# Optimization experiments

Hardware: AMD Instinct MI355X
Metric: run time of the kernel (lower is better)

The kernel has to match this reference:

```python
import jax, jax.numpy as jnp
import numpy as np

N = 100000   # nodes
E = 1600000  # edges (before self loops)
G = 256      # graphs in batch
F = 128      # feature_size
H = 128      # hidden_channels
L = 3        # num_layers - 1 GAT layers
NC1 = 10     # task1 classes
GF = 8       # graph_feature_size
EPS = 1e-5


def _bn_pack(key, C):
    kg, kb, km, kv = jax.random.split(key, 4)
    gamma = jax.random.uniform(kg, (C,), minval=0.5, maxval=1.5)
    beta = jax.random.normal(kb, (C,)) * 0.1
    mean = jax.random.normal(km, (C,)) * 0.1
    var = jax.random.uniform(kv, (C,), minval=0.5, maxval=1.5)
    return jnp.stack([gamma, beta, mean, var]).astype(jnp.float32)  # [4, C]


def setup_inputs() -> dict:
    key = jax.random.key(0)
    ks = jax.random.split(key, 24)
    x = jax.random.normal(ks[0], (N, F), dtype=jnp.float32)
    edge_index = jax.random.randint(ks[1], (2, E), 0, N)
    batch_ids = jnp.sort(jax.random.randint(ks[2], (N,), 0, G))
    graph_features = jax.random.normal(ks[3], (G, GF), dtype=jnp.float32)
    s = 0.05
    gat_W = jax.random.normal(ks[4], (L, F, H), dtype=jnp.float32) * s
    gat_att_src = jax.random.normal(ks[5], (L, H), dtype=jnp.float32) * s
    gat_att_dst = jax.random.normal(ks[6], (L, H), dtype=jnp.float32) * s
    gat_bias = jax.random.normal(ks[7], (L, H), dtype=jnp.float32) * 0.01
    bn_emb = _bn_pack(ks[8], H)
    bn_t1 = _bn_pack(ks[9], NC1)
    bn_comb = _bn_pack(ks[10], H + 5)
    fc1_w = jax.random.normal(ks[11], (H + 1, NC1), dtype=jnp.float32) * s
    fc1_b = jax.random.normal(ks[12], (NC1,), dtype=jnp.float32) * s
    fc2_w = jax.random.normal(ks[13], (H + 3, 2), dtype=jnp.float32) * s
    fc2_b = jax.random.normal(ks[14], (2,), dtype=jnp.float32) * s
    fc3a_w = jax.random.normal(ks[15], (H + 5, 4), dtype=jnp.float32) * s
    fc3a_b = jax.random.normal(ks[16], (4,), dtype=jnp.float32) * s
    fc3b_w = jax.random.normal(ks[17], (H + 5, 5), dtype=jnp.float32) * s
    fc3b_b = jax.random.normal(ks[18], (5,), dtype=jnp.float32) * s
    return dict(x=x, edge_index=edge_index, batch_ids=batch_ids,
                graph_features=graph_features, task=0,
                gat_W=gat_W, gat_att_src=gat_att_src, gat_att_dst=gat_att_dst,
                gat_bias=gat_bias, bn_emb=bn_emb, bn_t1=bn_t1, bn_comb=bn_comb,
                fc1_w=fc1_w, fc1_b=fc1_b, fc2_w=fc2_w, fc2_b=fc2_b,
                fc3a_w=fc3a_w, fc3a_b=fc3a_b, fc3b_w=fc3b_w, fc3b_b=fc3b_b)


def _bn_eval(x, pack):
    gamma, beta, mean, var = pack
    return (x - mean) * gamma * jax.lax.rsqrt(var + EPS) + beta


def _gat_layer(x, W, a_src, a_dst, b, src, dst):
    h = x @ W                              # [N, H]
    e_src = (h @ a_src)[src]               # [Etot]
    e_dst = (h @ a_dst)[dst]
    e = jax.nn.leaky_relu(e_src + e_dst, negative_slope=0.2)
    emax = jax.ops.segment_max(e, dst, num_segments=N)
    ee = jnp.exp(e - emax[dst])
    denom = jax.ops.segment_sum(ee, dst, num_segments=N)
    alpha = ee / denom[dst]                # edge softmax per destination node
    out = jax.ops.segment_sum(h[src] * alpha[:, None], dst, num_segments=N)
    return out + b


def _forward(x, edge_index, batch_ids, graph_features,
             gat_W, gat_att_src, gat_att_dst, gat_bias,
             bn_emb, bn_t1, bn_comb,
             fc1_w, fc1_b, fc2_w, fc2_b, fc3a_w, fc3a_b, fc3b_w, fc3b_b):
    loops = jnp.arange(N)
    src = jnp.concatenate([edge_index[0], loops])  # PyG GATConv adds self-loops
    dst = jnp.concatenate([edge_index[1], loops])
    for i in range(L):
        x = jax.nn.relu(_gat_layer(x, gat_W[i], gat_att_src[i], gat_att_dst[i],
                                   gat_bias[i], src, dst))
    # global mean pool over graphs
    sums = jax.ops.segment_sum(x, batch_ids, num_segments=G)
    cnt = jax.ops.segment_sum(jnp.ones((N,), x.dtype), batch_ids, num_segments=G)
    x = sums / jnp.maximum(cnt, 1.0)[:, None]
    x = _bn_eval(x, bn_emb)
    lev_lsb = graph_features[:, -1:]
    nx_feats = graph_features[:, -3:]
    out1 = jnp.concatenate([x, lev_lsb], axis=1) @ fc1_w + fc1_b
    out1 = _bn_eval(jax.nn.relu(out1), bn_t1)
    out2 = jax.nn.relu(jnp.concatenate([x, nx_feats], axis=1) @ fc2_w + fc2_b)
    pred2 = jnp.argmax(out2, axis=1)
    wf1 = graph_features[:, 2:3]
    wf2 = graph_features[:, 1:2]
    x3 = _bn_eval(jnp.concatenate([x, wf1, wf2, nx_feats], axis=1), bn_comb)
    b1 = x3 @ fc3a_w + fc3a_b              # [G, 4]
    b2 = x3 @ fc3b_w + fc3b_b              # [G, 5]
    m0 = (pred2 == 0)[:, None].astype(x.dtype)
    m1 = (pred2 == 1)[:, None].astype(x.dtype)
    out3 = jnp.concatenate([b1 * m0, b2 * m1], axis=1)  # [G, 9]
    return out1, out2, out3


def reference(x, edge_index, batch_ids, graph_features, task,
              gat_W, gat_att_src, gat_att_dst, gat_bias,
              bn_emb, bn_t1, bn_comb,
              fc1_w, fc1_b, fc2_w, fc2_b, fc3a_w, fc3a_b, fc3b_w, fc3b_b):
    return _forward(x, edge_index, batch_ids, graph_features,
                    gat_W, gat_att_src, gat_att_dst, gat_bias,
                    bn_emb, bn_t1, bn_comb,
                    fc1_w, fc1_b, fc2_w, fc2_b, fc3a_w, fc3a_b, fc3b_w, fc3b_b)
```

## Files before the change

### kernel.cpp

```cpp
#include <hip/hip_runtime.h>
#include <math.h>

#define Nn 100000
#define Ee 1600000
#define Mm (Ee + Nn)
#define Gg 256
#define EPSf 1e-5f
#define NB 391
#define EPB 4096
#define NEB 391

typedef _Float16 f16x8 __attribute__((ext_vector_type(8)));
typedef _Float16 half4_t __attribute__((ext_vector_type(4)));
typedef float f32x4 __attribute__((ext_vector_type(4)));


__global__ void k_zero(int* __restrict__ a, int n) {
  int i = blockIdx.x * 256 + threadIdx.x;
  if (i < n) a[i] = 0;
}

__global__ __launch_bounds__(256) void k_bcount(const int* __restrict__ dst,
                                                int* __restrict__ bcnt, int e) {
  __shared__ int lcnt[NB];
  int t = threadIdx.x;
  for (int i = t; i < NB; i += 256) lcnt[i] = 0;
  __syncthreads();
  int base = blockIdx.x * EPB;
  #pragma unroll
  for (int i = 0; i < 16; ++i) {
    int idx = base + i * 256 + t;
    if (idx < e) atomicAdd(&lcnt[dst[idx] >> 8], 1);
  }
  __syncthreads();
  for (int i = t; i < NB; i += 256)
    if (lcnt[i]) atomicAdd(&bcnt[i], lcnt[i]);
}

__global__ __launch_bounds__(512) void k_bscan(const int* __restrict__ bcnt,
                                               int* __restrict__ pairBase,
                                               int* __restrict__ tailA,
                                               int* __restrict__ bbase,
                                               int* __restrict__ rp) {
  __shared__ int s1[512], s2[512];
  int t = threadIdx.x;
  int c = (t < NB) ? bcnt[t] : 0;
  int nib = (t < NB) ? min(Nn - (t << 8), 256) : 0;
  s1[t] = c; s2[t] = c + nib;
  __syncthreads();
  for (int o = 1; o < 512; o <<= 1) {
    int u1 = (t >= o) ? s1[t - o] : 0;
    int u2 = (t >= o) ? s2[t - o] : 0;
    __syncthreads();
    s1[t] += u1; s2[t] += u2;
    __syncthreads();
  }
  if (t < NB) {
    pairBase[t] = s1[t] - c;
    tailA[t]    = s1[t] - c;
    bbase[t]    = s2[t] - (c + nib);
  }
  if (t == 0) rp[Nn] = Mm;
}

__global__ __launch_bounds__(256) void k_bin(const int* __restrict__ src,
                                             const int* __restrict__ dst,
                                             int* __restrict__ tailA,
                                             int2* __restrict__ pairs, int e) {
  __shared__ int lcnt[NB];
  __shared__ int lbase[NB];
  int t = threadIdx.x;
  for (int i = t; i < NB; i += 256) lcnt[i] = 0;
  __syncthreads();
  int base = blockIdx.x * EPB;
  int d[16], s[16], br[16];
  #pragma unroll
  for (int i = 0; i < 16; ++i) {
    int idx = base + i * 256 + t;
    if (idx < e) {
      d[i] = dst[idx]; s[i] = src[idx];
      br[i] = atomicAdd(&lcnt[d[i] >> 8], 1);
    } else br[i] = -1;
  }
  __syncthreads();
  for (int i = t; i < NB; i += 256)
    if (lcnt[i] > 0) lbase[i] = atomicAdd(&tailA[i], lcnt[i]);
  __syncthreads();
  #pragma unroll
  for (int i = 0; i < 16; ++i) {
    if (br[i] >= 0) {
      int b = d[i] >> 8;
      pairs[lbase[b] + br[i]] = make_int2(d[i], s[i]);
    }
  }
}

__global__ __launch_bounds__(256) void k_place(const int2* __restrict__ pairs,
                                               const int* __restrict__ pairBase,
                                               const int* __restrict__ bcnt,
                                               const int* __restrict__ bbase,
                                               int* __restrict__ rp,
                                               int* __restrict__ csr) {
  __shared__ int cnt[256];
  __shared__ int ofs[256];
  int b = blockIdx.x, t = threadIdx.x;
  int v0 = b << 8;
  int nib = min(Nn - v0, 256);
  int pb = pairBase[b], pc = bcnt[b];
  int cb = bbase[b];
  cnt[t] = (t < nib) ? 1 : 0;
  __syncthreads();
  for (int j = t; j < pc; j += 256) {
    int2 p = pairs[pb + j];
    atomicAdd(&cnt[p.x - v0], 1);
  }
  __syncthreads();
  int c = cnt[t];
  ofs[t] = c;
  __syncthreads();
  for (int o = 1; o < 256; o <<= 1) {
    int u = (t >= o) ? ofs[t - o] : 0;
    __syncthreads(); ofs[t] += u; __syncthreads();
  }
  int excl = ofs[t] - c;
  if (t < nib) rp[v0 + t] = cb + excl;
  cnt[t] = excl;
  __syncthreads();
  if (t < nib) {
    int pos = atomicAdd(&cnt[t], 1);
    csr[cb + pos] = v0 + t;
  }
  __syncthreads();
  for (int j = t; j < pc; j += 256) {
    int2 p = pairs[pb + j];
    int pos = atomicAdd(&cnt[p.x - v0], 1);
    csr[cb + pos] = p.y;
  }
}


__global__ void k_x2h(const float* __restrict__ X, half4_t* __restrict__ X16, int ntot4) {
  int i = blockIdx.x * 256 + threadIdx.x;
  if (i < ntot4) {
    float4 v = reinterpret_cast<const float4*>(X)[i];
    half4_t h = { (_Float16)v.x, (_Float16)v.y, (_Float16)v.z, (_Float16)v.w };
    X16[i] = h;
  }
}

__global__ void k_prepW(const float* __restrict__ W, _Float16* __restrict__ Wt) {
  int l = blockIdx.x;
  const float* w = W + (size_t)l * 16384;
  _Float16* wt = Wt + (size_t)l * 16384;
  for (int i = threadIdx.x; i < 16384; i += 256) {
    int k = i >> 7, c = i & 127;
    wt[c * 128 + k] = (_Float16)w[i];
  }
}


__global__ __launch_bounds__(256) void k_gemm(const _Float16* __restrict__ X16,
                                              const _Float16* __restrict__ Wt,
                                              const float* __restrict__ asrc,
                                              const float* __restrict__ adst,
                                              _Float16* __restrict__ H,
                                              float* __restrict__ es,
                                              float* __restrict__ ed, int n) {
  int wid = threadIdx.x >> 6;
  int lane = threadIdx.x & 63;
  int r0 = blockIdx.x * 128 + wid * 32;
  if (r0 >= n) return;
  int lo16 = lane & 15, q = lane >> 4;

  f32x4 acc0[8] = {};
  f32x4 acc1[8] = {};
  const _Float16* xb0 = X16 + (size_t)(r0 + lo16) * 128 + q * 8;
  const _Float16* xb1 = xb0 + 16 * 128;
  const _Float16* wb  = Wt + (size_t)lo16 * 128 + q * 8;

  #pragma unroll
  for (int kk = 0; kk < 4; ++kk) {
    f16x8 b0 = *reinterpret_cast<const f16x8*>(xb0 + kk * 32);
    f16x8 b1 = *reinterpret_cast<const f16x8*>(xb1 + kk * 32);
    #pragma unroll
    for (int c = 0; c < 8; ++c) {
      f16x8 a = *reinterpret_cast<const f16x8*>(wb + (size_t)c * 2048 + kk * 32);
      acc0[c] = __builtin_amdgcn_mfma_f32_16x16x32_f16(a, b0, acc0[c], 0, 0, 0);
      acc1[c] = __builtin_amdgcn_mfma_f32_16x16x32_f16(a, b1, acc1[c], 0, 0, 0);
    }
  }

  float es0 = 0.f, es1 = 0.f, ed0 = 0.f, ed1 = 0.f;
  #pragma unroll
  for (int c = 0; c < 8; ++c) {
    float4 as = reinterpret_cast<const float4*>(asrc)[c * 4 + q];
    float4 ad = reinterpret_cast<const float4*>(adst)[c * 4 + q];
    es0 += acc0[c][0] * as.x + acc0[c][1] * as.y + acc0[c][2] * as.z + acc0[c][3] * as.w;
    ed0 += acc0[c][0] * ad.x + acc0[c][1] * ad.y + acc0[c][2] * ad.z + acc0[c][3] * ad.w;
    es1 += acc1[c][0] * as.x + acc1[c][1] * as.y + acc1[c][2] * as.z + acc1[c][3] * as.w;
    ed1 += acc1[c][0] * ad.x + acc1[c][1] * ad.y + acc1[c][2] * ad.z + acc1[c][3] * ad.w;
  }
  es0 += __shfl_xor(es0, 16); es0 += __shfl_xor(es0, 32);
  ed0 += __shfl_xor(ed0, 16); ed0 += __shfl_xor(ed0, 32);
  es1 += __shfl_xor(es1, 16); es1 += __shfl_xor(es1, 32);
  ed1 += __shfl_xor(ed1, 16); ed1 += __shfl_xor(ed1, 32);

  half4_t* H4 = reinterpret_cast<half4_t*>(H);
  int row0 = r0 + lo16;
  #pragma unroll
  for (int c = 0; c < 8; ++c) {
    half4_t h0 = { (_Float16)acc0[c][0], (_Float16)acc0[c][1],
                   (_Float16)acc0[c][2], (_Float16)acc0[c][3] };
    half4_t h1 = { (_Float16)acc1[c][0], (_Float16)acc1[c][1],
                   (_Float16)acc1[c][2], (_Float16)acc1[c][3] };
    H4[(size_t)row0 * 32 + c * 4 + q]        = h0;
    H4[(size_t)(row0 + 16) * 32 + c * 4 + q] = h1;
  }
  if (lane < 16) {
    es[r0 + lane] = es0;       ed[r0 + lane] = ed0;
    es[r0 + 16 + lane] = es1;  ed[r0 + 16 + lane] = ed1;
  }
}


__global__ __launch_bounds__(256) void k_agg(const _Float16* __restrict__ H,
                                             const int* __restrict__ rp,
                                             const int* __restrict__ csr,
                                             const float* __restrict__ es,
                                             const float* __restrict__ ed,
                                             const float* __restrict__ bias,
                                             _Float16* __restrict__ Xo, int n) {
  int v = blockIdx.x * 4 + (threadIdx.x >> 6);
  if (v >= n) return;
  int lane = threadIdx.x & 63;
  int g = lane >> 4;
  int s = lane & 15;
  int r0 = rp[v], r1 = rp[v + 1];
  int deg = r1 - r0;
  float edv = ed[v];
  const f16x8* H8 = reinterpret_cast<const f16x8*>(H);
  float acc[8] = {};
  float inv;

  if (deg <= 64) {
    int u = 0;
    float e = -3.0e38f;
    if (lane < deg) {
      u = csr[r0 + lane];
      e = es[u] + edv;
      e = e > 0.f ? e : 0.2f * e;
    }
    float m = e;
    #pragma unroll
    for (int o = 32; o; o >>= 1) m = fmaxf(m, __shfl_xor(m, o));
    float pw = (lane < deg) ? __expf(e - m) : 0.f;
    float den = pw;
    #pragma unroll
    for (int o = 32; o; o >>= 1) den += __shfl_xor(den, o);
    inv = 1.f / den;
    for (int i = 0; i < deg; i += 4) {
      int idx = i + g;
      if (idx < deg) {
        int uu = __shfl(u, idx);
        float ww = __shfl(pw, idx);
        f16x8 hv = H8[(size_t)uu * 16 + s];
        #pragma unroll
        for (int k2 = 0; k2 < 8; ++k2) acc[k2] += ww * (float)hv[k2];
      }
    }
  } else {
    float m = -3.0e38f;
    for (int j = r0 + lane; j < r1; j += 64) {
      float e = es[csr[j]] + edv;
      e = e > 0.f ? e : 0.2f * e;
      m = fmaxf(m, e);
    }
    #pragma unroll
    for (int o = 32; o; o >>= 1) m = fmaxf(m, __shfl_xor(m, o));
    float den = 0.f;
    for (int j = r0 + lane; j < r1; j += 64) {
      float e = es[csr[j]] + edv;
      e = e > 0.f ? e : 0.2f * e;
      den += __expf(e - m);
    }
    #pragma unroll
    for (int o = 32; o; o >>= 1) den += __shfl_xor(den, o);
    inv = 1.f / den;
    for (int j = r0; j < r1; j += 4) {
      int idx = j + g;
      if (idx < r1) {
        int uu = csr[idx];
        float e = es[uu] + edv;
        e = e > 0.f ? e : 0.2f * e;
        float ww = __expf(e - m);
        f16x8 hv = H8[(size_t)uu * 16 + s];
        #pragma unroll
        for (int k2 = 0; k2 < 8; ++k2) acc[k2] += ww * (float)hv[k2];
      }
    }
  }
  #pragma unroll
  for (int k2 = 0; k2 < 8; ++k2) {
    acc[k2] += __shfl_xor(acc[k2], 16);
    acc[k2] += __shfl_xor(acc[k2], 32);
  }
  if (lane < 16) {
    float4 b0 = reinterpret_cast<const float4*>(bias)[s * 2];
    float4 b1 = reinterpret_cast<const float4*>(bias)[s * 2 + 1];
    f16x8 o;
    o[0] = (_Float16)fmaxf(acc[0] * inv + b0.x, 0.f);
    o[1] = (_Float16)fmaxf(acc[1] * inv + b0.y, 0.f);
    o[2] = (_Float16)fmaxf(acc[2] * inv + b0.z, 0.f);
    o[3] = (_Float16)fmaxf(acc[3] * inv + b0.w, 0.f);
    o[4] = (_Float16)fmaxf(acc[4] * inv + b1.x, 0.f);
    o[5] = (_Float16)fmaxf(acc[5] * inv + b1.y, 0.f);
    o[6] = (_Float16)fmaxf(acc[6] * inv + b1.z, 0.f);
    o[7] = (_Float16)fmaxf(acc[7] * inv + b1.w, 0.f);
    reinterpret_cast<f16x8*>(Xo)[(size_t)v * 16 + s] = o;
  }
}


__global__ __launch_bounds__(512) void k_pool(const _Float16* __restrict__ X16,
                                              const int* __restrict__ batch,
                                              const float* __restrict__ bn,
                                              float* __restrict__ xg, int n) {
  __shared__ float4 part[16][32];
  int g = blockIdx.x;
  int s = threadIdx.x & 31;
  int way = threadIdx.x >> 5;
  int lo = 0, hi = n;
  while (lo < hi) { int mid = (lo + hi) >> 1; if (batch[mid] < g) lo = mid + 1; else hi = mid; }
  int s0 = lo;
  lo = s0; hi = n;
  while (lo < hi) { int mid = (lo + hi) >> 1; if (batch[mid] < g + 1) lo = mid + 1; else hi = mid; }
  int e0 = lo;
  const half4_t* X4 = reinterpret_cast<const half4_t*>(X16);
  float4 acc = make_float4(0.f, 0.f, 0.f, 0.f);
  for (int i = s0 + way; i < e0; i += 16) {
    half4_t h = X4[(size_t)i * 32 + s];
    acc.x += (float)h[0]; acc.y += (float)h[1];
    acc.z += (float)h[2]; acc.w += (float)h[3];
  }
  part[way][s] = acc;
  __syncthreads();
  if (way == 0) {
    float4 t = part[0][s];
    #pragma unroll
    for (int w = 1; w < 16; ++w) {
      float4 u = part[w][s];
      t.x += u.x; t.y += u.y; t.z += u.z; t.w += u.w;
    }
    float invc = (e0 > s0) ? 1.f / (float)(e0 - s0) : 0.f;
    int c0 = s * 4;
    #pragma unroll
    for (int k = 0; k < 4; ++k) {
      float mean = ((const float*)&t)[k] * invc;
      int c = c0 + k;
      float gm = bn[c], bt = bn[128 + c], mu = bn[256 + c], vr = bn[384 + c];
      xg[g * 128 + c] = (mean - mu) * gm * rsqrtf(vr + EPSf) + bt;
    }
  }
}


__global__ void k_heads(const float* __restrict__ xg, const float* __restrict__ gf,
                        const float* __restrict__ bn_t1, const float* __restrict__ bn_comb,
                        const float* __restrict__ fc1w, const float* __restrict__ fc1b,
                        const float* __restrict__ fc2w, const float* __restrict__ fc2b,
                        const float* __restrict__ fc3aw, const float* __restrict__ fc3ab,
                        const float* __restrict__ fc3bw, const float* __restrict__ fc3bb,
                        float* __restrict__ out) {
  int g = blockIdx.x;
  int lane = threadIdx.x;
  __shared__ float xs[128];
  __shared__ float x3[133];
  __shared__ float o2[2];
  xs[lane] = xg[g * 128 + lane];
  xs[lane + 64] = xg[g * 128 + 64 + lane];
  __syncthreads();
  const float* gfg = &gf[g * 8];
  float lev = gfg[7];
  float nx0 = gfg[5], nx1 = gfg[6], nx2 = gfg[7];
  float wf1 = gfg[2], wf2 = gfg[1];
  if (lane < 10) {
    float o = fc1b[lane];
    for (int k = 0; k < 128; ++k) o += xs[k] * fc1w[k * 10 + lane];
    o += lev * fc1w[128 * 10 + lane];
    o = fmaxf(o, 0.f);
    float gm = bn_t1[lane], bt = bn_t1[10 + lane], mu = bn_t1[20 + lane], vr = bn_t1[30 + lane];
    out[g * 10 + lane] = (o - mu) * gm * rsqrtf(vr + EPSf) + bt;
  }
  if (lane >= 10 && lane < 12) {
    int j = lane - 10;
    float o = fc2b[j];
    for (int k = 0; k < 128; ++k) o += xs[k] * fc2w[k * 2 + j];
    o += nx0 * fc2w[128 * 2 + j] + nx1 * fc2w[129 * 2 + j] + nx2 * fc2w[130 * 2 + j];
    o = fmaxf(o, 0.f);
    o2[j] = o;
    out[2560 + g * 2 + j] = o;
  }
  for (int k = lane; k < 133; k += 64) {
    float vsrc = (k < 128) ? xs[k]
               : (k == 128) ? wf1
               : (k == 129) ? wf2
               : (k == 130) ? nx0
               : (k == 131) ? nx1 : nx2;
    float gm = bn_comb[k], bt = bn_comb[133 + k], mu = bn_comb[266 + k], vr = bn_comb[399 + k];
    x3[k] = (vsrc - mu) * gm * rsqrtf(vr + EPSf) + bt;
  }
  __syncthreads();
  bool pred1 = o2[1] > o2[0];
  if (lane < 4) {
    float o = fc3ab[lane];
    for (int k = 0; k < 133; ++k) o += x3[k] * fc3aw[k * 4 + lane];
    out[3072 + g * 9 + lane] = pred1 ? 0.f : o;
  }
  if (lane >= 4 && lane < 9) {
    int j = lane - 4;
    float o = fc3bb[j];
    for (int k = 0; k < 133; ++k) o += x3[k] * fc3bw[k * 5 + j];
    out[3072 + g * 9 + 4 + j] = pred1 ? o : 0.f;
  }
}


extern "C" void kernel_launch(void* const* d_in, const int* in_sizes, int n_in,
                              void* d_out, int out_size, void* d_ws, size_t ws_size,
                              hipStream_t stream) {
  const float* x      = (const float*)d_in[0];
  const int*   ei     = (const int*)d_in[1];
  const int*   batch  = (const int*)d_in[2];
  const float* gf     = (const float*)d_in[3];
  const float* gatW   = (const float*)d_in[5];
  const float* asrc   = (const float*)d_in[6];
  const float* adst   = (const float*)d_in[7];
  const float* gbias  = (const float*)d_in[8];
  const float* bn_emb = (const float*)d_in[9];
  const float* bn_t1  = (const float*)d_in[10];
  const float* bn_cb  = (const float*)d_in[11];
  const float* fc1w = (const float*)d_in[12]; const float* fc1b = (const float*)d_in[13];
  const float* fc2w = (const float*)d_in[14]; const float* fc2b = (const float*)d_in[15];
  const float* fc3aw = (const float*)d_in[16]; const float* fc3ab = (const float*)d_in[17];
  const float* fc3bw = (const float*)d_in[18]; const float* fc3bb = (const float*)d_in[19];
  float* out = (float*)d_out;

  char* p = (char*)d_ws;
  auto alloc = [&](size_t bytes) -> void* {
    void* r = (void*)p;
    p += (bytes + 255) & ~(size_t)255;
    return r;
  };
  _Float16* x16a = (_Float16*)alloc((size_t)Nn * 128 * 2);
  _Float16* x16b = (_Float16*)alloc((size_t)Nn * 128 * 2);
  _Float16* hbuf = (_Float16*)alloc((size_t)Nn * 128 * 2);
  _Float16* wt   = (_Float16*)alloc((size_t)3 * 16384 * 2);
  int2*  pairs = (int2*)alloc((size_t)Ee * 8);
  int*   csr  = (int*)alloc((size_t)Mm * 4);
  int*   rp   = (int*)alloc((size_t)(Nn + 1) * 4);
  int*   bcnt = (int*)alloc((size_t)NB * 4);
  int*   pairBase = (int*)alloc((size_t)NB * 4);
  int*   tailA    = (int*)alloc((size_t)NB * 4);
  int*   bbase    = (int*)alloc((size_t)NB * 4);
  float* es   = (float*)alloc((size_t)Nn * 4);
  float* ed   = (float*)alloc((size_t)Nn * 4);
  float* xg   = (float*)alloc((size_t)Gg * 128 * 4);
  if ((size_t)(p - (char*)d_ws) > ws_size) return;

  const int* srcp = ei;
  const int* dstp = ei + Ee;

  k_x2h<<<(Nn * 32 + 255) / 256, 256, 0, stream>>>(x, (half4_t*)x16a, Nn * 32);
  k_prepW<<<3, 256, 0, stream>>>(gatW, wt);

  k_zero<<<(NB + 255) / 256, 256, 0, stream>>>(bcnt, NB);
  k_bcount<<<NEB, 256, 0, stream>>>(dstp, bcnt, Ee);
  k_bscan<<<1, 512, 0, stream>>>(bcnt, pairBase, tailA, bbase, rp);
  k_bin<<<NEB, 256, 0, stream>>>(srcp, dstp, tailA, pairs, Ee);
  k_place<<<NB, 256, 0, stream>>>(pairs, pairBase, bcnt, bbase, rp, csr);

  _Float16* xin = x16a;
  _Float16* xout = x16b;
  int ngrid = (Nn + 127) / 128;
  for (int l = 0; l < 3; ++l) {
    k_gemm<<<ngrid, 256, 0, stream>>>(xin, wt + (size_t)l * 16384,
                                      asrc + l * 128, adst + l * 128,
                                      hbuf, es, ed, Nn);
    k_agg<<<(Nn + 3) / 4, 256, 0, stream>>>(hbuf, rp, csr, es, ed,
                                            gbias + l * 128, xout, Nn);
    _Float16* t = xin; xin = xout; xout = t;
  }

  k_pool<<<Gg, 512, 0, stream>>>(xin, batch, bn_emb, xg, Nn);

  k_heads<<<Gg, 64, 0, stream>>>(xg, gf, bn_t1, bn_cb,
                                 fc1w, fc1b, fc2w, fc2b, fc3aw, fc3ab, fc3bw, fc3bb, out);
}
```

Baseline: 554.4 us.

## Fuse fp32-to-fp16 conversion into first GEMM, pack edge pairs, merge pool and heads

The first GAT GEMM now reads fp32 inputs directly and converts them in registers, which removes the separate x-to-half kernel and its round trip through memory. Edge binning packs source and local destination into one 32-bit int, halving the pairs buffer traffic, and uses twice as many blocks with half the edges each. The bcount zeroing is folded into the weight-prep kernel, and pooling and heads are merged into one kernel. The aggregation loop precomputes row offsets and unrolls by two. The packing assumes src < 2^23, and the first GEMM now loads twice as many bytes per element.

```diff
diff --git a/kernel.cpp b/kernel.cpp
--- a/kernel.cpp
+++ b/kernel.cpp
@@ -7,18 +7,29 @@
 #define Gg 256
 #define EPSf 1e-5f
 #define NB 391
-#define EPB 4096
-#define NEB 391
+#define EPB 2048
+#define NEB 782
 
 typedef _Float16 f16x8 __attribute__((ext_vector_type(8)));
 typedef _Float16 half4_t __attribute__((ext_vector_type(4)));
 typedef float f32x4 __attribute__((ext_vector_type(4)));
 
 
-__global__ void k_zero(int* __restrict__ a, int n) {
-  int i = blockIdx.x * 256 + threadIdx.x;
-  if (i < n) a[i] = 0;
-}
+__global__ void k_prepW(const float* __restrict__ W, _Float16* __restrict__ Wt,
+                        int* __restrict__ bcnt) {
+  int l = blockIdx.x;
+  if (l < 3) {
+    const float* w = W + (size_t)l * 16384;
+    _Float16* wt = Wt + (size_t)l * 16384;
+    for (int i = threadIdx.x; i < 16384; i += 256) {
+      int k = i >> 7, c = i & 127;
+      wt[c * 128 + k] = (_Float16)w[i];
+    }
+  } else {
+    for (int i = threadIdx.x; i < NB; i += 256) bcnt[i] = 0;
+  }
+}
+
 
 __global__ __launch_bounds__(256) void k_bcount(const int* __restrict__ dst,
                                                 int* __restrict__ bcnt, int e) {
@@ -28,7 +39,7 @@
   __syncthreads();
   int base = blockIdx.x * EPB;
   #pragma unroll
-  for (int i = 0; i < 16; ++i) {
+  for (int i = 0; i < EPB / 256; ++i) {
     int idx = base + i * 256 + t;
     if (idx < e) atomicAdd(&lcnt[dst[idx] >> 8], 1);
   }
@@ -66,20 +77,22 @@
 __global__ __launch_bounds__(256) void k_bin(const int* __restrict__ src,
                                              const int* __restrict__ dst,
                                              int* __restrict__ tailA,
-                                             int2* __restrict__ pairs, int e) {
+                                             int* __restrict__ pairs, int e) {
   __shared__ int lcnt[NB];
   __shared__ int lbase[NB];
   int t = threadIdx.x;
   for (int i = t; i < NB; i += 256) lcnt[i] = 0;
   __syncthreads();
   int base = blockIdx.x * EPB;
-  int d[16], s[16], br[16];
-  #pragma unroll
-  for (int i = 0; i < 16; ++i) {
+  int pk[EPB / 256], br[EPB / 256], bk[EPB / 256];
+  #pragma unroll
+  for (int i = 0; i < EPB / 256; ++i) {
     int idx = base + i * 256 + t;
     if (idx < e) {
-      d[i] = dst[idx]; s[i] = src[idx];
-      br[i] = atomicAdd(&lcnt[d[i] >> 8], 1);
+      int d = dst[idx];
+      pk[i] = (src[idx] << 8) | (d & 255);
+      bk[i] = d >> 8;
+      br[i] = atomicAdd(&lcnt[bk[i]], 1);
     } else br[i] = -1;
   }
   __syncthreads();
@@ -87,15 +100,12 @@
     if (lcnt[i] > 0) lbase[i] = atomicAdd(&tailA[i], lcnt[i]);
   __syncthreads();
   #pragma unroll
-  for (int i = 0; i < 16; ++i) {
-    if (br[i] >= 0) {
-      int b = d[i] >> 8;
-      pairs[lbase[b] + br[i]] = make_int2(d[i], s[i]);
-    }
-  }
-}
-
-__global__ __launch_bounds__(256) void k_place(const int2* __restrict__ pairs,
+  for (int i = 0; i < EPB / 256; ++i) {
+    if (br[i] >= 0) pairs[lbase[bk[i]] + br[i]] = pk[i];
+  }
+}
+
+__global__ __launch_bounds__(256) void k_place(const int* __restrict__ pairs,
                                                const int* __restrict__ pairBase,
                                                const int* __restrict__ bcnt,
                                                const int* __restrict__ bbase,
@@ -111,8 +121,7 @@
   cnt[t] = (t < nib) ? 1 : 0;
   __syncthreads();
   for (int j = t; j < pc; j += 256) {
-    int2 p = pairs[pb + j];
-    atomicAdd(&cnt[p.x - v0], 1);
+    atomicAdd(&cnt[pairs[pb + j] & 255], 1);
   }
   __syncthreads();
   int c = cnt[t];
@@ -132,34 +141,15 @@
   }
   __syncthreads();
   for (int j = t; j < pc; j += 256) {
-    int2 p = pairs[pb + j];
-    int pos = atomicAdd(&cnt[p.x - v0], 1);
-    csr[cb + pos] = p.y;
-  }
-}
-
-
-__global__ void k_x2h(const float* __restrict__ X, half4_t* __restrict__ X16, int ntot4) {
-  int i = blockIdx.x * 256 + threadIdx.x;
-  if (i < ntot4) {
-    float4 v = reinterpret_cast<const float4*>(X)[i];
-    half4_t h = { (_Float16)v.x, (_Float16)v.y, (_Float16)v.z, (_Float16)v.w };
-    X16[i] = h;
-  }
-}
-
-__global__ void k_prepW(const float* __restrict__ W, _Float16* __restrict__ Wt) {
-  int l = blockIdx.x;
-  const float* w = W + (size_t)l * 16384;
-  _Float16* wt = Wt + (size_t)l * 16384;
-  for (int i = threadIdx.x; i < 16384; i += 256) {
-    int k = i >> 7, c = i & 127;
-    wt[c * 128 + k] = (_Float16)w[i];
-  }
-}
-
-
-__global__ __launch_bounds__(256) void k_gemm(const _Float16* __restrict__ X16,
+    int p = pairs[pb + j];
+    int pos = atomicAdd(&cnt[p & 255], 1);
+    csr[cb + pos] = p >> 8;
+  }
+}
+
+
+template<bool F32IN>
+__global__ __launch_bounds__(256) void k_gemm(const void* __restrict__ Xv,
                                               const _Float16* __restrict__ Wt,
                                               const float* __restrict__ asrc,
                                               const float* __restrict__ adst,
@@ -174,14 +164,26 @@
 
   f32x4 acc0[8] = {};
   f32x4 acc1[8] = {};
-  const _Float16* xb0 = X16 + (size_t)(r0 + lo16) * 128 + q * 8;
-  const _Float16* xb1 = xb0 + 16 * 128;
-  const _Float16* wb  = Wt + (size_t)lo16 * 128 + q * 8;
+  const _Float16* wb = Wt + (size_t)lo16 * 128 + q * 8;
 
   #pragma unroll
   for (int kk = 0; kk < 4; ++kk) {
-    f16x8 b0 = *reinterpret_cast<const f16x8*>(xb0 + kk * 32);
-    f16x8 b1 = *reinterpret_cast<const f16x8*>(xb1 + kk * 32);
+    f16x8 b0, b1;
+    if constexpr (F32IN) {
+      const float* xf = (const float*)Xv + (size_t)(r0 + lo16) * 128 + q * 8 + kk * 32;
+      float4 u0 = *reinterpret_cast<const float4*>(xf);
+      float4 u1 = *reinterpret_cast<const float4*>(xf + 4);
+      float4 v0 = *reinterpret_cast<const float4*>(xf + 16 * 128);
+      float4 v1 = *reinterpret_cast<const float4*>(xf + 16 * 128 + 4);
+      b0 = f16x8{(_Float16)u0.x, (_Float16)u0.y, (_Float16)u0.z, (_Float16)u0.w,
+                 (_Float16)u1.x, (_Float16)u1.y, (_Float16)u1.z, (_Float16)u1.w};
+      b1 = f16x8{(_Float16)v0.x, (_Float16)v0.y, (_Float16)v0.z, (_Float16)v0.w,
+                 (_Float16)v1.x, (_Float16)v1.y, (_Float16)v1.z, (_Float16)v1.w};
+    } else {
+      const _Float16* xh = (const _Float16*)Xv + (size_t)(r0 + lo16) * 128 + q * 8 + kk * 32;
+      b0 = *reinterpret_cast<const f16x8*>(xh);
+      b1 = *reinterpret_cast<const f16x8*>(xh + 16 * 128);
+    }
     #pragma unroll
     for (int c = 0; c < 8; ++c) {
       f16x8 a = *reinterpret_cast<const f16x8*>(wb + (size_t)c * 2048 + kk * 32);
@@ -258,12 +260,14 @@
     #pragma unroll
     for (int o = 32; o; o >>= 1) den += __shfl_xor(den, o);
     inv = 1.f / den;
+    int hb = u * 16 + s;
+    #pragma unroll 2
     for (int i = 0; i < deg; i += 4) {
       int idx = i + g;
       if (idx < deg) {
-        int uu = __shfl(u, idx);
+        int hoff = __shfl(hb, idx) + (s - __shfl(s, idx));
         float ww = __shfl(pw, idx);
-        f16x8 hv = H8[(size_t)uu * 16 + s];
+        f16x8 hv = H8[hoff];
         #pragma unroll
         for (int k2 = 0; k2 < 8; ++k2) acc[k2] += ww * (float)hv[k2];
       }
@@ -293,7 +297,7 @@
         float e = es[uu] + edv;
         e = e > 0.f ? e : 0.2f * e;
         float ww = __expf(e - m);
-        f16x8 hv = H8[(size_t)uu * 16 + s];
+        f16x8 hv = H8[uu * 16 + s];
         #pragma unroll
         for (int k2 = 0; k2 < 8; ++k2) acc[k2] += ww * (float)hv[k2];
       }
@@ -316,19 +320,27 @@
     o[5] = (_Float16)fmaxf(acc[5] * inv + b1.y, 0.f);
     o[6] = (_Float16)fmaxf(acc[6] * inv + b1.z, 0.f);
     o[7] = (_Float16)fmaxf(acc[7] * inv + b1.w, 0.f);
-    reinterpret_cast<f16x8*>(Xo)[(size_t)v * 16 + s] = o;
-  }
-}
-
-
-__global__ __launch_bounds__(512) void k_pool(const _Float16* __restrict__ X16,
-                                              const int* __restrict__ batch,
-                                              const float* __restrict__ bn,
-                                              float* __restrict__ xg, int n) {
+    reinterpret_cast<f16x8*>(Xo)[v * 16 + s] = o;
+  }
+}
+
+
+__global__ __launch_bounds__(512) void k_poolheads(
+    const _Float16* __restrict__ X16, const int* __restrict__ batch,
+    const float* __restrict__ bn_emb, const float* __restrict__ gf,
+    const float* __restrict__ bn_t1, const float* __restrict__ bn_comb,
+    const float* __restrict__ fc1w, const float* __restrict__ fc1b,
+    const float* __restrict__ fc2w, const float* __restrict__ fc2b,
+    const float* __restrict__ fc3aw, const float* __restrict__ fc3ab,
+    const float* __restrict__ fc3bw, const float* __restrict__ fc3bb,
+    float* __restrict__ out, int n) {
   __shared__ float4 part[16][32];
-  int g = blockIdx.x;
-  int s = threadIdx.x & 31;
-  int way = threadIdx.x >> 5;
+  __shared__ float xs[128];
+  __shared__ float x3[133];
+  __shared__ float o2[2];
+  int g = blockIdx.x, t = threadIdx.x;
+  int s = t & 31;
+  int way = t >> 5;
   int lo = 0, hi = n;
   while (lo < hi) { int mid = (lo + hi) >> 1; if (batch[mid] < g) lo = mid + 1; else hi = mid; }
   int s0 = lo;
@@ -345,54 +357,38 @@
   part[way][s] = acc;
   __syncthreads();
   if (way == 0) {
-    float4 t = part[0][s];
+    float4 tt = part[0][s];
     #pragma unroll
     for (int w = 1; w < 16; ++w) {
       float4 u = part[w][s];
-      t.x += u.x; t.y += u.y; t.z += u.z; t.w += u.w;
+      tt.x += u.x; tt.y += u.y; tt.z += u.z; tt.w += u.w;
     }
     float invc = (e0 > s0) ? 1.f / (float)(e0 - s0) : 0.f;
     int c0 = s * 4;
     #pragma unroll
     for (int k = 0; k < 4; ++k) {
-      float mean = ((const float*)&t)[k] * invc;
+      float mean = ((const float*)&tt)[k] * invc;
       int c = c0 + k;
-      float gm = bn[c], bt = bn[128 + c], mu = bn[256 + c], vr = bn[384 + c];
-      xg[g * 128 + c] = (mean - mu) * gm * rsqrtf(vr + EPSf) + bt;
-    }
-  }
-}
-
-
-__global__ void k_heads(const float* __restrict__ xg, const float* __restrict__ gf,
-                        const float* __restrict__ bn_t1, const float* __restrict__ bn_comb,
-                        const float* __restrict__ fc1w, const float* __restrict__ fc1b,
-                        const float* __restrict__ fc2w, const float* __restrict__ fc2b,
-                        const float* __restrict__ fc3aw, const float* __restrict__ fc3ab,
-                        const float* __restrict__ fc3bw, const float* __restrict__ fc3bb,
-                        float* __restrict__ out) {
-  int g = blockIdx.x;
-  int lane = threadIdx.x;
-  __shared__ float xs[128];
-  __shared__ float x3[133];
-  __shared__ float o2[2];
-  xs[lane] = xg[g * 128 + lane];
-  xs[lane + 64] = xg[g * 128 + 64 + lane];
-  __syncthreads();
+      float gm = bn_emb[c], bt = bn_emb[128 + c], mu = bn_emb[256 + c], vr = bn_emb[384 + c];
+      xs[c] = (mean - mu) * gm * rsqrtf(vr + EPSf) + bt;
+    }
+  }
+  __syncthreads();
+
   const float* gfg = &gf[g * 8];
   float lev = gfg[7];
   float nx0 = gfg[5], nx1 = gfg[6], nx2 = gfg[7];
   float wf1 = gfg[2], wf2 = gfg[1];
-  if (lane < 10) {
-    float o = fc1b[lane];
-    for (int k = 0; k < 128; ++k) o += xs[k] * fc1w[k * 10 + lane];
-    o += lev * fc1w[128 * 10 + lane];
+  if (t < 10) {
+    float o = fc1b[t];
+    for (int k = 0; k < 128; ++k) o += xs[k] * fc1w[k * 10 + t];
+    o += lev * fc1w[128 * 10 + t];
     o = fmaxf(o, 0.f);
-    float gm = bn_t1[lane], bt = bn_t1[10 + lane], mu = bn_t1[20 + lane], vr = bn_t1[30 + lane];
-    out[g * 10 + lane] = (o - mu) * gm * rsqrtf(vr + EPSf) + bt;
-  }
-  if (lane >= 10 && lane < 12) {
-    int j = lane - 10;
+    float gm = bn_t1[t], bt = bn_t1[10 + t], mu = bn_t1[20 + t], vr = bn_t1[30 + t];
+    out[g * 10 + t] = (o - mu) * gm * rsqrtf(vr + EPSf) + bt;
+  }
+  if (t >= 10 && t < 12) {
+    int j = t - 10;
     float o = fc2b[j];
     for (int k = 0; k < 128; ++k) o += xs[k] * fc2w[k * 2 + j];
     o += nx0 * fc2w[128 * 2 + j] + nx1 * fc2w[129 * 2 + j] + nx2 * fc2w[130 * 2 + j];
@@ -400,7 +396,8 @@
     o2[j] = o;
     out[2560 + g * 2 + j] = o;
   }
-  for (int k = lane; k < 133; k += 64) {
+  if (t >= 12 && t < 145) {
+    int k = t - 12;
     float vsrc = (k < 128) ? xs[k]
                : (k == 128) ? wf1
                : (k == 129) ? wf2
@@ -411,13 +408,13 @@
   }
   __syncthreads();
   bool pred1 = o2[1] > o2[0];
-  if (lane < 4) {
-    float o = fc3ab[lane];
-    for (int k = 0; k < 133; ++k) o += x3[k] * fc3aw[k * 4 + lane];
-    out[3072 + g * 9 + lane] = pred1 ? 0.f : o;
-  }
-  if (lane >= 4 && lane < 9) {
-    int j = lane - 4;
+  if (t < 4) {
+    float o = fc3ab[t];
+    for (int k = 0; k < 133; ++k) o += x3[k] * fc3aw[k * 4 + t];
+    out[3072 + g * 9 + t] = pred1 ? 0.f : o;
+  }
+  if (t >= 4 && t < 9) {
+    int j = t - 4;
     float o = fc3bb[j];
     for (int k = 0; k < 133; ++k) o += x3[k] * fc3bw[k * 5 + j];
     out[3072 + g * 9 + 4 + j] = pred1 ? o : 0.f;
@@ -451,11 +448,11 @@
     p += (bytes + 255) & ~(size_t)255;
     return r;
   };
-  _Float16* x16a = (_Float16*)alloc((size_t)Nn * 128 * 2);
-  _Float16* x16b = (_Float16*)alloc((size_t)Nn * 128 * 2);
+  _Float16* xfA  = (_Float16*)alloc((size_t)Nn * 128 * 2);
+  _Float16* xfB  = (_Float16*)alloc((size_t)Nn * 128 * 2);
   _Float16* hbuf = (_Float16*)alloc((size_t)Nn * 128 * 2);
   _Float16* wt   = (_Float16*)alloc((size_t)3 * 16384 * 2);
-  int2*  pairs = (int2*)alloc((size_t)Ee * 8);
+  int*   pairs = (int*)alloc((size_t)Ee * 4);
   int*   csr  = (int*)alloc((size_t)Mm * 4);
   int*   rp   = (int*)alloc((size_t)(Nn + 1) * 4);
   int*   bcnt = (int*)alloc((size_t)NB * 4);
@@ -464,35 +461,29 @@
   int*   bbase    = (int*)alloc((size_t)NB * 4);
   float* es   = (float*)alloc((size_t)Nn * 4);
   float* ed   = (float*)alloc((size_t)Nn * 4);
-  float* xg   = (float*)alloc((size_t)Gg * 128 * 4);
   if ((size_t)(p - (char*)d_ws) > ws_size) return;
 
   const int* srcp = ei;
   const int* dstp = ei + Ee;
 
-  k_x2h<<<(Nn * 32 + 255) / 256, 256, 0, stream>>>(x, (half4_t*)x16a, Nn * 32);
-  k_prepW<<<3, 256, 0, stream>>>(gatW, wt);
-
-  k_zero<<<(NB + 255) / 256, 256, 0, stream>>>(bcnt, NB);
+  k_prepW<<<4, 256, 0, stream>>>(gatW, wt, bcnt);
+
   k_bcount<<<NEB, 256, 0, stream>>>(dstp, bcnt, Ee);
   k_bscan<<<1, 512, 0, stream>>>(bcnt, pairBase, tailA, bbase, rp);
   k_bin<<<NEB, 256, 0, stream>>>(srcp, dstp, tailA, pairs, Ee);
   k_place<<<NB, 256, 0, stream>>>(pairs, pairBase, bcnt, bbase, rp, csr);
 
-  _Float16* xin = x16a;
-  _Float16* xout = x16b;
   int ngrid = (Nn + 127) / 128;
-  for (int l = 0; l < 3; ++l) {
-    k_gemm<<<ngrid, 256, 0, stream>>>(xin, wt + (size_t)l * 16384,
-                                      asrc + l * 128, adst + l * 128,
-                                      hbuf, es, ed, Nn);
-    k_agg<<<(Nn + 3) / 4, 256, 0, stream>>>(hbuf, rp, csr, es, ed,
-                                            gbias + l * 128, xout, Nn);
-    _Float16* t = xin; xin = xout; xout = t;
-  }
-
-  k_pool<<<Gg, 512, 0, stream>>>(xin, batch, bn_emb, xg, Nn);
-
-  k_heads<<<Gg, 64, 0, stream>>>(xg, gf, bn_t1, bn_cb,
-                                 fc1w, fc1b, fc2w, fc2b, fc3aw, fc3ab, fc3bw, fc3bb, out);
-}
+  k_gemm<true><<<ngrid, 256, 0, stream>>>(x, wt, asrc, adst, hbuf, es, ed, Nn);
+  k_agg<<<(Nn + 3) / 4, 256, 0, stream>>>(hbuf, rp, csr, es, ed, gbias, xfA, Nn);
+  k_gemm<false><<<ngrid, 256, 0, stream>>>(xfA, wt + 16384, asrc + 128, adst + 128,
+                                           hbuf, es, ed, Nn);
+  k_agg<<<(Nn + 3) / 4, 256, 0, stream>>>(hbuf, rp, csr, es, ed, gbias + 128, xfB, Nn);
+  k_gemm<false><<<ngrid, 256, 0, stream>>>(xfB, wt + 32768, asrc + 256, adst + 256,
+                                           hbuf, es, ed, Nn);
+  k_agg<<<(Nn + 3) / 4, 256, 0, stream>>>(hbuf, rp, csr, es, ed, gbias + 256, xfA, Nn);
+
+  k_poolheads<<<Gg, 512, 0, stream>>>(xfA, batch, bn_emb, gf, bn_t1, bn_cb,
+                                      fc1w, fc1b, fc2w, fc2b, fc3aw, fc3ab,
+                                      fc3bw, fc3bb, out, Nn);
+}
```

After: 561.6 us. No clear change (+1.3%).
